# Kernel optimization log

Hardware: AMD Instinct MI355X
Metric: run time of the kernel (lower is better)

## Reference

```python
import jax, jax.numpy as jnp
import numpy as np

DIM = 1024
HEADS = 16
DIM_HEAD = 64
INNER = HEADS * DIM_HEAD  # 1024
EPS = 1e-5


def setup_inputs() -> dict:
    key = jax.random.key(0)
    ks = jax.random.split(key, 8)
    B, N = 4, 2048
    s = 0.02
    return {
        "query": jax.random.normal(ks[0], (B, N, DIM), jnp.float32),
        "key_": jax.random.normal(ks[1], (B, N, DIM), jnp.float32),
        "value": jax.random.normal(ks[2], (B, N, DIM), jnp.float32),
        "Wq": jax.random.normal(ks[3], (DIM, INNER), jnp.float32) * s,
        "Wk": jax.random.normal(ks[4], (DIM, INNER), jnp.float32) * s,
        "Wv": jax.random.normal(ks[5], (DIM, INNER), jnp.float32) * s,
        "Wo": jax.random.normal(ks[6], (INNER, DIM), jnp.float32) * s,
        "bo": jnp.zeros((DIM,), jnp.float32),
        "gamma": jnp.ones((DIM,), jnp.float32),
        "beta": jnp.zeros((DIM,), jnp.float32),
    }


def reference(query, key_, value, Wq, Wk, Wv, Wo, bo, gamma, beta):
    B, N, _ = query.shape
    scale = DIM_HEAD ** (-0.5)
    # project and split heads: [B, H, N, Dh]
    q = (query @ Wq).reshape(B, N, HEADS, DIM_HEAD).transpose(0, 2, 1, 3)
    k = (key_ @ Wk).reshape(B, N, HEADS, DIM_HEAD).transpose(0, 2, 1, 3)
    v = (value @ Wv).reshape(B, N, HEADS, DIM_HEAD).transpose(0, 2, 1, 3)
    dots = jnp.einsum("bhnd,bhmd->bhnm", q, k) * scale  # [B,H,N,N]
    attn = jax.nn.softmax(dots, axis=-1)
    out = jnp.einsum("bhnm,bhmd->bhnd", attn, v)
    out = out.transpose(0, 2, 1, 3).reshape(B, N, INNER)
    out = out @ Wo + bo  # dropout p=0.0 is identity
    # LayerNorm over last dim
    mu = out.mean(-1, keepdims=True)
    var = ((out - mu) ** 2).mean(-1, keepdims=True)
    normed = (out - mu) * jax.lax.rsqrt(var + EPS) * gamma + beta
    return normed + query
```

## Files before the change

kernel.cpp:

```cpp
#include <hip/hip_runtime.h>
#include <stdint.h>

#define K_DIM 1024
#define B_SZ 4
#define N_SEQ 2048
#define HEADS 16
#define DH 64
#define M_TOT (B_SZ * N_SEQ)

typedef __bf16 bf16x8 __attribute__((ext_vector_type(8)));
typedef __bf16 bf16x4 __attribute__((ext_vector_type(4)));
typedef float f32x4 __attribute__((ext_vector_type(4)));

typedef const uint32_t __attribute__((address_space(1))) gas_u32;
typedef uint32_t __attribute__((address_space(3))) las_u32;

#define CE_SCALE 0.1803368801f

__device__ __forceinline__ uint16_t f2bf(float f) {
  uint32_t u = __float_as_uint(f);
  u += 0x7FFFu + ((u >> 16) & 1u);
  return (uint16_t)(u >> 16);
}

__device__ __forceinline__ void gld_lds16(const uint16_t* g, uint16_t* lds) {
  __builtin_amdgcn_global_load_lds((gas_u32*)g, (las_u32*)lds, 16, 0, 0);
}

__global__ __launch_bounds__(256) void conv_bf16_k(const float* __restrict__ s0,
                                                   const float* __restrict__ s1,
                                                   const float* __restrict__ s2,
                                                   uint16_t* __restrict__ dstbase, int n4) {
  const int z = blockIdx.y;
  const float* src = (z == 0) ? s0 : (z == 1) ? s1 : s2;
  uint16_t* dst = dstbase + (size_t)z * M_TOT * K_DIM;
  int i = blockIdx.x * blockDim.x + threadIdx.x;
  if (i < n4) {
    float4 v = ((const float4*)src)[i];
    ushort4 o;
    o.x = f2bf(v.x); o.y = f2bf(v.y); o.z = f2bf(v.z); o.w = f2bf(v.w);
    ((ushort4*)dst)[i] = o;
  }
}

__global__ __launch_bounds__(256) void transpose_conv(const float* __restrict__ s0,
                                                      const float* __restrict__ s1,
                                                      const float* __restrict__ s2,
                                                      const float* __restrict__ s3,
                                                      uint16_t* __restrict__ dstbase) {
  __shared__ float tile[32][33];
  const int z = blockIdx.z;
  const float* src = (z == 0) ? s0 : (z == 1) ? s1 : (z == 2) ? s2 : s3;
  uint16_t* dst = dstbase + (size_t)z * 1024 * 1024;
  const int tx = threadIdx.x, ty = threadIdx.y;
  const int bx = blockIdx.x * 32, by = blockIdx.y * 32;
#pragma unroll
  for (int i = 0; i < 32; i += 8)
    tile[ty + i][tx] = src[(size_t)(by + ty + i) * 1024 + bx + tx];
  __syncthreads();
#pragma unroll
  for (int i = 0; i < 32; i += 8)
    dst[(size_t)(bx + ty + i) * 1024 + by + tx] = f2bf(tile[tx][ty + i]);
}

template <int MODE>
__global__ __launch_bounds__(256, 2) void gemm_bf16(const uint16_t* __restrict__ A,
                                                    const uint16_t* __restrict__ BT,
                                                    void* __restrict__ Cout,
                                                    const float* __restrict__ bias) {
  __shared__ __align__(16) uint16_t As[128 * 32];
  __shared__ __align__(16) uint16_t Bs[128 * 32];
  const int tid = threadIdx.x;
  const int wave = tid >> 6, lane = tid & 63;
  const int g = lane >> 4, c16 = lane & 15;
  const int m0 = blockIdx.y * 128, n0 = blockIdx.x * 128;
  const int wr = wave >> 1, wc = wave & 1;
  int z = 0;
  float scale = 1.f;
  if (MODE == 3) {
    z = blockIdx.z;
    A += (size_t)z * M_TOT * K_DIM;
    BT += (size_t)z * 1024 * 1024;
    scale = (z == 0) ? CE_SCALE : 1.f;
  }

  const f32x4 fzero = {0.f, 0.f, 0.f, 0.f};
  f32x4 acc[4][4];
#pragma unroll
  for (int i = 0; i < 4; ++i)
#pragma unroll
    for (int j = 0; j < 4; ++j) acc[i][j] = fzero;

  const int srow = wave * 32 + (lane >> 2);
  const int scol = (lane & 3) * 8;
  const uint16_t* ag0 = A + (size_t)(m0 + srow) * K_DIM + scol;
  const uint16_t* ag1 = A + (size_t)(m0 + srow + 16) * K_DIM + scol;
  const uint16_t* bg0 = BT + (size_t)(n0 + srow) * K_DIM + scol;
  const uint16_t* bg1 = BT + (size_t)(n0 + srow + 16) * K_DIM + scol;
  uint16_t* la0 = &As[(wave * 32) * 32];
  uint16_t* la1 = &As[(wave * 32 + 16) * 32];
  uint16_t* lb0 = &Bs[(wave * 32) * 32];
  uint16_t* lb1 = &Bs[(wave * 32 + 16) * 32];

  for (int kt = 0; kt < K_DIM / 32; ++kt) {
    __syncthreads();
    gld_lds16(ag0 + kt * 32, la0);
    gld_lds16(ag1 + kt * 32, la1);
    gld_lds16(bg0 + kt * 32, lb0);
    gld_lds16(bg1 + kt * 32, lb1);
    __syncthreads();
    bf16x8 avec[4], bvec[4];
#pragma unroll
    for (int i = 0; i < 4; ++i)
      avec[i] = *(const bf16x8*)&As[(wr * 64 + i * 16 + c16) * 32 + g * 8];
#pragma unroll
    for (int j = 0; j < 4; ++j)
      bvec[j] = *(const bf16x8*)&Bs[(wc * 64 + j * 16 + c16) * 32 + g * 8];
#pragma unroll
    for (int i = 0; i < 4; ++i)
#pragma unroll
      for (int j = 0; j < 4; ++j)
        acc[i][j] = __builtin_amdgcn_mfma_f32_16x16x32_bf16(avec[i], bvec[j], acc[i][j], 0, 0, 0);
  }

#pragma unroll
  for (int i = 0; i < 4; ++i) {
#pragma unroll
    for (int j = 0; j < 4; ++j) {
      const int col = n0 + wc * 64 + j * 16 + c16;
      if (MODE == 3 && z == 2) {
        const int h = col >> 6, d = col & 63;
        const int row0 = m0 + wr * 64 + i * 16 + g * 4;
        const int b = row0 >> 11, n = row0 & 2047;
        ushort4 o;
        o.x = f2bf(acc[i][j][0]); o.y = f2bf(acc[i][j][1]);
        o.z = f2bf(acc[i][j][2]); o.w = f2bf(acc[i][j][3]);
        *(ushort4*)&((uint16_t*)Cout)[(size_t)2 * M_TOT * 1024 +
                                      (((size_t)(b * HEADS + h)) * DH + d) * N_SEQ + n] = o;
      } else {
#pragma unroll
        for (int r = 0; r < 4; ++r) {
          const int row = m0 + wr * 64 + i * 16 + g * 4 + r;
          if (MODE == 3) {
            const int b = row >> 11, n = row & 2047;
            const int h = col >> 6, d = col & 63;
            ((uint16_t*)Cout)[(size_t)z * M_TOT * 1024 +
                              (((size_t)(b * HEADS + h)) * N_SEQ + n) * DH + d] =
                f2bf(acc[i][j][r] * scale);
          } else {
            ((float*)Cout)[(size_t)row * 1024 + col] = acc[i][j][r] + bias[col];
          }
        }
      }
    }
  }
}

__global__ __launch_bounds__(256, 2) void attention_k(const uint16_t* __restrict__ qm,
                                                      const uint16_t* __restrict__ km,
                                                      const uint16_t* __restrict__ vtm,
                                                      uint16_t* __restrict__ om) {
  __shared__ __align__(16) uint16_t Ks[64 * 64];
  __shared__ __align__(16) uint16_t Vs[64 * 64];
  __shared__ __align__(16) uint16_t Pt[4][64 * 64];
  const int tid = threadIdx.x;
  const int wave = tid >> 6, lane = tid & 63;
  const int g = lane >> 4, c16 = lane & 15;
  const int bh = blockIdx.y, b = bh >> 4, h = bh & 15;
  const int q0 = blockIdx.x * 256 + wave * 64;

  const uint16_t* qbase = qm + (size_t)bh * N_SEQ * DH;
  const uint16_t* kbase = km + (size_t)bh * N_SEQ * DH;
  const uint16_t* vbase = vtm + (size_t)bh * DH * N_SEQ;

  bf16x8 qf[4][2];
#pragma unroll
  for (int qc = 0; qc < 4; ++qc) {
    const uint16_t* qp = qbase + (size_t)(q0 + qc * 16 + c16) * DH + g * 8;
    qf[qc][0] = *(const bf16x8*)qp;
    qf[qc][1] = *(const bf16x8*)(qp + 32);
  }

  const f32x4 fz = {0.f, 0.f, 0.f, 0.f};
  f32x4 oacc[4][4];
#pragma unroll
  for (int qc = 0; qc < 4; ++qc)
#pragma unroll
    for (int jt = 0; jt < 4; ++jt) oacc[qc][jt] = fz;
  float l[4] = {0.f, 0.f, 0.f, 0.f};

  uint16_t* ptw = Pt[wave];
  const int sw = c16 & 7;

  const int ch = tid & 7;
  const int krow0 = tid >> 3, krow1 = (256 + tid) >> 3;
  const int kdst0 = krow0 * 64 + ((ch ^ (krow0 & 7)) << 3);
  const int kdst1 = krow1 * 64 + ((ch ^ (krow1 & 7)) << 3);

  uint4 kp0, kp1, vp0, vp1;
  kp0 = *(const uint4*)&kbase[(size_t)tid * 8];
  kp1 = *(const uint4*)&kbase[(size_t)(256 + tid) * 8];
  vp0 = *(const uint4*)&vbase[(size_t)krow0 * N_SEQ + ch * 8];
  vp1 = *(const uint4*)&vbase[(size_t)krow1 * N_SEQ + ch * 8];
  *(uint4*)&Ks[kdst0] = kp0;
  *(uint4*)&Ks[kdst1] = kp1;
  *(uint4*)&Vs[kdst0] = vp0;
  *(uint4*)&Vs[kdst1] = vp1;
  __syncthreads();

  for (int t = 0; t < N_SEQ / 64; ++t) {
    if (t < N_SEQ / 64 - 1) {
      const size_t ko = (size_t)(t + 1) * 4096;
      const int vc = (t + 1) * 64;
      kp0 = *(const uint4*)&kbase[ko + (size_t)tid * 8];
      kp1 = *(const uint4*)&kbase[ko + (size_t)(256 + tid) * 8];
      vp0 = *(const uint4*)&vbase[(size_t)krow0 * N_SEQ + vc + ch * 8];
      vp1 = *(const uint4*)&vbase[(size_t)krow1 * N_SEQ + vc + ch * 8];
    }

#pragma unroll
    for (int kt = 0; kt < 4; ++kt) {
      const int krow = kt * 16 + c16;
      bf16x8 kf0 = *(const bf16x8*)&Ks[krow * 64 + ((g ^ sw) << 3)];
      bf16x8 kf1 = *(const bf16x8*)&Ks[krow * 64 + (((4 + g) ^ sw) << 3)];
      const int pcol = (((kt * 2 + (g >> 1)) ^ sw) << 3) + (g & 1) * 4;
#pragma unroll
      for (int qc = 0; qc < 4; ++qc) {
        f32x4 z = fz;
        z = __builtin_amdgcn_mfma_f32_16x16x32_bf16(kf0, qf[qc][0], z, 0, 0, 0);
        z = __builtin_amdgcn_mfma_f32_16x16x32_bf16(kf1, qf[qc][1], z, 0, 0, 0);
        const float p0 = __builtin_amdgcn_exp2f(z[0]);
        const float p1 = __builtin_amdgcn_exp2f(z[1]);
        const float p2 = __builtin_amdgcn_exp2f(z[2]);
        const float p3 = __builtin_amdgcn_exp2f(z[3]);
        l[qc] += (p0 + p1) + (p2 + p3);
        bf16x4 pk;
        pk[0] = (__bf16)p0; pk[1] = (__bf16)p1; pk[2] = (__bf16)p2; pk[3] = (__bf16)p3;
        *(bf16x4*)&ptw[(qc * 16 + c16) * 64 + pcol] = pk;
      }
    }

#pragma unroll
    for (int kc = 0; kc < 2; ++kc) {
      const int fcol = ((kc * 4 + g) ^ sw) << 3;
      bf16x8 pa[4];
#pragma unroll
      for (int qc = 0; qc < 4; ++qc)
        pa[qc] = *(const bf16x8*)&ptw[(qc * 16 + c16) * 64 + fcol];
#pragma unroll
      for (int jt = 0; jt < 4; ++jt) {
        bf16x8 vb = *(const bf16x8*)&Vs[(jt * 16 + c16) * 64 + fcol];
#pragma unroll
        for (int qc = 0; qc < 4; ++qc)
          oacc[qc][jt] = __builtin_amdgcn_mfma_f32_16x16x32_bf16(pa[qc], vb, oacc[qc][jt], 0, 0, 0);
      }
    }

    if (t < N_SEQ / 64 - 1) {
      __syncthreads();
      *(uint4*)&Ks[kdst0] = kp0;
      *(uint4*)&Ks[kdst1] = kp1;
      *(uint4*)&Vs[kdst0] = vp0;
      *(uint4*)&Vs[kdst1] = vp1;
      __syncthreads();
    }
  }

#pragma unroll
  for (int qc = 0; qc < 4; ++qc) {
    l[qc] += __shfl_xor(l[qc], 16);
    l[qc] += __shfl_xor(l[qc], 32);
  }

#pragma unroll
  for (int qc = 0; qc < 4; ++qc) {
#pragma unroll
    for (int r = 0; r < 4; ++r) {
      const float lr = __shfl(l[qc], g * 4 + r, 16);
      const float inv = 1.f / lr;
      const int row = q0 + qc * 16 + g * 4 + r;
      const size_t base = ((size_t)b * N_SEQ + row) * 1024 + h * 64;
#pragma unroll
      for (int jt = 0; jt < 4; ++jt)
        om[base + jt * 16 + c16] = f2bf(oacc[qc][jt][r] * inv);
    }
  }
}

__global__ __launch_bounds__(256) void ln_res_k(const float* __restrict__ proj,
                                                const float* __restrict__ query,
                                                const float* __restrict__ gamma,
                                                const float* __restrict__ beta,
                                                float* __restrict__ out) {
  const int row = blockIdx.x;
  const int tid = threadIdx.x;
  const size_t base = (size_t)row * 1024 + tid * 4;
  float4 v = *(const float4*)(proj + base);
  float s = v.x + v.y + v.z + v.w;
  float s2 = v.x * v.x + v.y * v.y + v.z * v.z + v.w * v.w;
#pragma unroll
  for (int off = 1; off < 64; off <<= 1) {
    s += __shfl_xor(s, off);
    s2 += __shfl_xor(s2, off);
  }
  __shared__ float red[8];
  const int wave = tid >> 6, lane = tid & 63;
  if (lane == 0) { red[wave] = s; red[4 + wave] = s2; }
  __syncthreads();
  s = red[0] + red[1] + red[2] + red[3];
  s2 = red[4] + red[5] + red[6] + red[7];
  const float mu = s * (1.f / 1024.f);
  const float var = fmaxf(s2 * (1.f / 1024.f) - mu * mu, 0.f);
  const float rstd = rsqrtf(var + 1e-5f);
  float4 gq = *(const float4*)(gamma + tid * 4);
  float4 bq = *(const float4*)(beta + tid * 4);
  float4 qq = *(const float4*)(query + base);
  float4 o;
  o.x = (v.x - mu) * rstd * gq.x + bq.x + qq.x;
  o.y = (v.y - mu) * rstd * gq.y + bq.y + qq.y;
  o.z = (v.z - mu) * rstd * gq.z + bq.z + qq.z;
  o.w = (v.w - mu) * rstd * gq.w + bq.w + qq.w;
  *(float4*)(out + base) = o;
}

extern "C" void kernel_launch(void* const* d_in, const int* in_sizes, int n_in,
                              void* d_out, int out_size, void* d_ws, size_t ws_size,
                              hipStream_t stream) {
  (void)in_sizes; (void)n_in; (void)out_size; (void)ws_size;
  const float* query = (const float*)d_in[0];
  const float* key_ = (const float*)d_in[1];
  const float* value = (const float*)d_in[2];
  const float* Wq = (const float*)d_in[3];
  const float* Wk = (const float*)d_in[4];
  const float* Wv = (const float*)d_in[5];
  const float* Wo = (const float*)d_in[6];
  const float* bo = (const float*)d_in[7];
  const float* gamma = (const float*)d_in[8];
  const float* beta = (const float*)d_in[9];
  float* out = (float*)d_out;

  const size_t NELEM = (size_t)M_TOT * 1024;
  uint16_t* wsp = (uint16_t*)d_ws;
  uint16_t* WqT = wsp;
  uint16_t* WoT = WqT + 3 * 1024 * 1024;
  uint16_t* xq = WqT + 4 * 1024 * 1024;
  uint16_t* qb = xq + 3 * NELEM;
  uint16_t* attnO = xq;
  float* proj = (float*)(xq + NELEM);

  const int n4 = (int)(NELEM / 4);
  conv_bf16_k<<<dim3(8192, 3), 256, 0, stream>>>(query, key_, value, xq, n4);

  transpose_conv<<<dim3(32, 32, 4), dim3(32, 8), 0, stream>>>(Wq, Wk, Wv, Wo, WqT);

  gemm_bf16<3><<<dim3(8, 64, 3), 256, 0, stream>>>(xq, WqT, qb, nullptr);

  attention_k<<<dim3(N_SEQ / 256, 64), 256, 0, stream>>>(qb, qb + NELEM, qb + 2 * NELEM, attnO);

  gemm_bf16<1><<<dim3(8, 64), 256, 0, stream>>>(attnO, WoT, proj, bo);

  ln_res_k<<<8192, 256, 0, stream>>>(proj, query, gamma, beta, out);
}
```

Baseline: 365.0 us.

## Keep softmax probabilities in registers and feed PV via 16x16x16 MFMA

Removes the per-wave LDS staging buffer for the probability tile. The S=K·Q^T MFMA output layout is reused directly as the A operand of a 16x16x16 bf16 MFMA for the P·V product, so the LDS writes and reads of P are gone and LDS use drops. The trade is twice as many, smaller MFMA instructions for PV, and 8-byte V fragment loads replace 16-byte ones. The lower LDS footprint may also allow more blocks per CU.

```diff
diff --git a/kernel.cpp b/kernel.cpp
--- a/kernel.cpp
+++ b/kernel.cpp
@@ -11,6 +11,7 @@
 typedef __bf16 bf16x8 __attribute__((ext_vector_type(8)));
 typedef __bf16 bf16x4 __attribute__((ext_vector_type(4)));
 typedef float f32x4 __attribute__((ext_vector_type(4)));
+typedef short s16x4 __attribute__((ext_vector_type(4)));
 
 typedef const uint32_t __attribute__((address_space(1))) gas_u32;
 typedef uint32_t __attribute__((address_space(3))) las_u32;
@@ -25,6 +26,25 @@
 
 __device__ __forceinline__ void gld_lds16(const uint16_t* g, uint16_t* lds) {
   __builtin_amdgcn_global_load_lds((gas_u32*)g, (las_u32*)lds, 16, 0, 0);
+}
+
+#if defined(__has_builtin)
+#if __has_builtin(__builtin_amdgcn_mfma_f32_16x16x16bf16_1k)
+#define HAVE_MFMA16_BUILTIN 1
+#endif
+#endif
+
+__device__ __forceinline__ f32x4 mfma16(bf16x4 a, bf16x4 b, f32x4 c) {
+#ifdef HAVE_MFMA16_BUILTIN
+  return __builtin_amdgcn_mfma_f32_16x16x16bf16_1k(
+      __builtin_bit_cast(s16x4, a), __builtin_bit_cast(s16x4, b), c, 0, 0, 0);
+#else
+  f32x4 d;
+  asm("v_mfma_f32_16x16x16_bf16 %0, %1, %2, %3"
+      : "=v"(d)
+      : "v"(a), "v"(b), "v"(c));
+  return d;
+#endif
 }
 
 __global__ __launch_bounds__(256) void conv_bf16_k(const float* __restrict__ s0,
@@ -162,7 +182,6 @@
                                                       uint16_t* __restrict__ om) {
   __shared__ __align__(16) uint16_t Ks[64 * 64];
   __shared__ __align__(16) uint16_t Vs[64 * 64];
-  __shared__ __align__(16) uint16_t Pt[4][64 * 64];
   const int tid = threadIdx.x;
   const int wave = tid >> 6, lane = tid & 63;
   const int g = lane >> 4, c16 = lane & 15;
@@ -189,7 +208,6 @@
     for (int jt = 0; jt < 4; ++jt) oacc[qc][jt] = fz;
   float l[4] = {0.f, 0.f, 0.f, 0.f};
 
-  uint16_t* ptw = Pt[wave];
   const int sw = c16 & 7;
 
   const int ch = tid & 7;
@@ -223,7 +241,7 @@
       const int krow = kt * 16 + c16;
       bf16x8 kf0 = *(const bf16x8*)&Ks[krow * 64 + ((g ^ sw) << 3)];
       bf16x8 kf1 = *(const bf16x8*)&Ks[krow * 64 + (((4 + g) ^ sw) << 3)];
-      const int pcol = (((kt * 2 + (g >> 1)) ^ sw) << 3) + (g & 1) * 4;
+      bf16x4 pk[4];
 #pragma unroll
       for (int qc = 0; qc < 4; ++qc) {
         f32x4 z = fz;
@@ -234,25 +252,16 @@
         const float p2 = __builtin_amdgcn_exp2f(z[2]);
         const float p3 = __builtin_amdgcn_exp2f(z[3]);
         l[qc] += (p0 + p1) + (p2 + p3);
-        bf16x4 pk;
-        pk[0] = (__bf16)p0; pk[1] = (__bf16)p1; pk[2] = (__bf16)p2; pk[3] = (__bf16)p3;
-        *(bf16x4*)&ptw[(qc * 16 + c16) * 64 + pcol] = pk;
+        bf16x4 pq;
+        pq[0] = (__bf16)p0; pq[1] = (__bf16)p1; pq[2] = (__bf16)p2; pq[3] = (__bf16)p3;
+        pk[qc] = pq;
       }
-    }
-
-#pragma unroll
-    for (int kc = 0; kc < 2; ++kc) {
-      const int fcol = ((kc * 4 + g) ^ sw) << 3;
-      bf16x8 pa[4];
-#pragma unroll
-      for (int qc = 0; qc < 4; ++qc)
-        pa[qc] = *(const bf16x8*)&ptw[(qc * 16 + c16) * 64 + fcol];
 #pragma unroll
       for (int jt = 0; jt < 4; ++jt) {
-        bf16x8 vb = *(const bf16x8*)&Vs[(jt * 16 + c16) * 64 + fcol];
-#pragma unroll
-        for (int qc = 0; qc < 4; ++qc)
-          oacc[qc][jt] = __builtin_amdgcn_mfma_f32_16x16x32_bf16(pa[qc], vb, oacc[qc][jt], 0, 0, 0);
+        bf16x4 vb = *(const bf16x4*)&Vs[(jt * 16 + c16) * 64 +
+                                        (((kt * 2 + (g >> 1)) ^ sw) << 3) + (g & 1) * 4];
+#pragma unroll
+        for (int qc = 0; qc < 4; ++qc) oacc[qc][jt] = mfma16(pk[qc], vb, oacc[qc][jt]);
       }
     }
 
```

Result: no change. 360.8 us (-1.2%).
